# Kernel optimization log

Hardware: AMD Instinct MI355X
Metric: run time of the kernel (lower is better)

Reference implementation:

```python
import jax, jax.numpy as jnp
import numpy as np

BS, SEQ, DIM, L = 32, 256, 6, 400
NH, DM, DFF, DOUT = 2, 4, 16, 32
MAXA, ILEN = SEQ // 2 + 2, 20
THR, HW = 0.001, 2


def _layernorm(x, g, b):
    m = x.mean(-1, keepdims=True)
    v = ((x - m) ** 2).mean(-1, keepdims=True)
    return (x - m) * jax.lax.rsqrt(v + 1e-5) * g + b


def _get_max(t, ws):
    # non-overlapping window peak suppression: keep only per-window argmax value
    bs, Lt = t.shape
    nwin = Lt // ws
    w = t[:, :nwin * ws].reshape(bs, nwin, ws)
    oh = jax.nn.one_hot(jnp.argmax(w, axis=2), ws, dtype=t.dtype)
    return (w * oh).reshape(bs, nwin * ws)


def reference(x, imu_mask, imu_len, conv_w, conv_b, W_b1, b_b1, W_fc, b_fc,
              Wqkv, Wo, ln1_g, ln1_b, Wf1, bf1, Wf2, bf2, ln2_g, ln2_b,
              Wout, bout, Wd1, bd1, Wd2, bd2, Wa, ba):
    bs, seq, dim, l = x.shape
    N = bs * seq
    # --- CNN encoder: valid conv1d -> relu -> 2-bin mean pool -> (N,32,2) ---
    y = jax.lax.conv_general_dilated(x.reshape(N, dim, l), conv_w, (1,), 'VALID',
                                     dimension_numbers=('NCH', 'OIH', 'NCH'))
    y = jax.nn.relu(y + conv_b[None, :, None])  # (N,32,398)
    half = y.shape[-1] // 2
    pooled = jnp.stack([y[:, :, :half].mean(-1), y[:, :, half:2 * half].mean(-1)], -1)
    cnn_flat = pooled.reshape(N, -1)  # (N,64)
    bridge_out = jax.nn.sigmoid(cnn_flat @ W_b1 + b_b1)  # (N,4)
    # --- one-step forecasting loss -> data-dependent peaks ---
    forcast_in = bridge_out.reshape(bs, seq, DM)
    shft = jnp.pad(forcast_in, ((0, 0), (1, 0), (0, 0)))[:, :-1]
    fmask = jnp.ones_like(forcast_in).at[:, 0, :].set(0.0)
    fmask = (fmask * imu_mask[:, :, 0, 0][:, :, None]).reshape(N, DM)
    forcast = shft.reshape(N, DM) @ W_fc + b_fc
    floss = jnp.mean(jnp.square(forcast * fmask - forcast_in.reshape(N, DM) * fmask), axis=1)
    floss = floss.reshape(bs, seq)
    lmask = jnp.ones_like(floss).at[:, :2].set(0.0).at[:, -2:].set(0.0)
    floss = floss * ((floss > THR) * lmask)
    sel = _get_max(floss, 2 * HW)            # (bs,seq)
    sel2 = _get_max(sel[:, HW:], 2 * HW)     # (bs,seq-4)
    sel2 = jnp.pad(sel2, ((0, 0), (HW, 0)))
    if sel.shape[1] > sel2.shape[1]:
        sel2 = jnp.pad(sel2, ((0, 0), (0, HW)))
    seg_points = sel2 > 0
    last = jnp.clip(jnp.round(imu_len.astype(jnp.float32) / seq).astype(jnp.int32), 2, seq)
    # --- merge unit-length segments (vectorized equivalent of the while-loop) ---
    pos = jnp.arange(seq)
    point = seg_points & (pos[None] < last[:, None])
    bnd_next = jnp.pad(point, ((0, 0), (0, 1)))[:, 1:] | (pos[None] + 1 == last[:, None])
    kept = point & ~bnd_next                 # a boundary survives iff next segment len > 1
    seg_id = jnp.cumsum(kept, axis=1)
    valid_t = pos[None] < last[:, None]
    same = (seg_id[:, :, None] == seg_id[:, None, :]) & valid_t[:, :, None] & valid_t[:, None, :]
    attn_mask = jnp.where(same | jnp.eye(seq, dtype=bool)[None], 0.0, -jnp.inf)[:, None]
    # --- 1-layer post-norm transformer with block-diagonal mask ---
    hb = bridge_out.reshape(seq, bs, DM).transpose(1, 0, 2)  # faithful reshape order
    qkv = jnp.einsum('bsd,cde->cbse', hb, Wqkv)
    hd = DM // NH
    q, k, v = [t.reshape(bs, seq, NH, hd) for t in qkv]
    scores = jnp.einsum('bqhd,bkhd->bhqk', q, k) / np.sqrt(hd) + attn_mask
    attn = jax.nn.softmax(scores, axis=-1)
    ao = jnp.einsum('bhqk,bkhd->bqhd', attn, v).reshape(bs, seq, DM) @ Wo
    h1 = _layernorm(hb + ao, ln1_g, ln1_b)
    ff = jax.nn.relu(h1 @ Wf1 + bf1) @ Wf2 + bf2
    h2 = _layernorm(h1 + ff, ln2_g, ln2_b)
    tr_out = h2 @ Wout + bout                # (bs,seq,32)
    # --- per-segment atom embeddings, padded to MAXA slots ---
    n_kept = kept.sum(1)
    kp = jnp.sort(jnp.where(kept, pos[None], seq), axis=1)[:, :MAXA]
    a_idx = jnp.arange(MAXA)
    ends = jnp.where(a_idx[None] < n_kept[:, None], kp, last[:, None])
    starts = jnp.concatenate([jnp.zeros((bs, 1), ends.dtype), ends[:, :-1]], axis=1)
    atom_valid = (a_idx[None] <= n_kept[:, None]).astype(x.dtype)
    emb = jnp.take_along_axis(tr_out, jnp.clip(ends - 1, 0, seq - 1)[:, :, None], axis=1)
    atom_gen = (emb.reshape(-1, DOUT) @ Wa + ba).reshape(bs, MAXA, dim, ILEN)
    atom_gen = atom_gen * atom_valid[:, :, None, None]
    # --- per-segment nearest resample to ILEN via one batched gather ---
    xf = x.transpose(0, 2, 1, 3).reshape(bs, dim, seq * l)
    in_len = (ends - starts) * l
    idx = starts[:, :, None] * l + (jnp.arange(ILEN)[None, None] * in_len[:, :, None]) // ILEN
    idx = jnp.clip(idx, 0, seq * l - 1)
    seg_interp = xf[jnp.arange(bs)[:, None, None], :, idx]  # (bs,MAXA,ILEN,dim)
    seg_interp = seg_interp.transpose(0, 1, 3, 2) * atom_valid[:, :, None, None]
    # --- imu decoder ---
    imu_gen = (jax.nn.relu(bridge_out @ Wd1 + bd1) @ Wd2 + bd2).reshape(bs, seq, dim, l)
    return jnp.concatenate([imu_gen.ravel(), atom_gen.ravel(), seg_interp.ravel(),
                            forcast.ravel(), floss.ravel()])


def setup_inputs() -> dict:
    key = jax.random.key(0)
    ks = jax.random.split(key, 20)
    f32 = jnp.float32
    nrm = lambda k, s, sc: jax.random.normal(k, s, f32) * sc
    inp = {
        'x': nrm(ks[0], (BS, SEQ, DIM, L), 1.0),
        'imu_mask': jnp.ones((BS, SEQ, 1, 1), f32),
        'imu_len': jax.random.randint(ks[1], (BS,), SEQ * SEQ // 2, SEQ * SEQ),
        'conv_w': nrm(ks[2], (32, DIM, 3), 0.24),
        'conv_b': jnp.zeros((32,), f32),
        'W_b1': nrm(ks[3], (64, DM), 0.125),
        'b_b1': jnp.zeros((DM,), f32),
        'W_fc': nrm(ks[4], (DM, DM), 0.5),
        'b_fc': jnp.zeros((DM,), f32),
        'Wqkv': nrm(ks[5], (3, DM, DM), 0.5),
        'Wo': nrm(ks[6], (DM, DM), 0.5),
        'ln1_g': jnp.ones((DM,), f32), 'ln1_b': jnp.zeros((DM,), f32),
        'Wf1': nrm(ks[7], (DM, DFF), 0.5), 'bf1': jnp.zeros((DFF,), f32),
        'Wf2': nrm(ks[8], (DFF, DM), 0.25), 'bf2': jnp.zeros((DM,), f32),
        'ln2_g': jnp.ones((DM,), f32), 'ln2_b': jnp.zeros((DM,), f32),
        'Wout': nrm(ks[9], (DM, DOUT), 0.5), 'bout': jnp.zeros((DOUT,), f32),
        'Wd1': nrm(ks[10], (DM, 64), 0.5), 'bd1': jnp.zeros((64,), f32),
        'Wd2': nrm(ks[11], (64, DIM * L), 0.125), 'bd2': jnp.zeros((DIM * L,), f32),
        'Wa': nrm(ks[12], (DOUT, DIM * ILEN), 0.18), 'ba': jnp.zeros((DIM * ILEN,), f32),
    }
    return inp
```

## Files before the change

kernel.cpp:

```cpp
#include <hip/hip_runtime.h>
#include <hip/hip_bf16.h>
#include <math.h>

#define OFF_IMU  0
#define OFF_ATOM 19660800
#define OFF_SEG  20160000
#define OFF_FC   20659200
#define OFF_FL   20691968

#define WS_BRIDGE 0
#define WS_TR     32768
#define WS_ENDS   303104
#define WS_STARTS 307264
#define WS_NK     311424

static __device__ __forceinline__ int imin(int a, int b) { return a < b ? a : b; }
static __device__ __forceinline__ int imax(int a, int b) { return a > b ? a : b; }

typedef __attribute__((ext_vector_type(8))) short bf16x8;
typedef __attribute__((ext_vector_type(4))) float f32x4;
union AF { uint32_t u[4]; bf16x8 v; };

static __device__ __forceinline__ uint32_t pack_hilo(float x)
{
    __hip_bfloat16 h = __float2bfloat16(x);
    const float hf = __bfloat162float(h);
    __hip_bfloat16 lo = __float2bfloat16(x - hf);
    const uint32_t hb = *(const unsigned short*)&h;
    const uint32_t lb = *(const unsigned short*)&lo;
    return hb | (lb << 16);
}

__global__ __launch_bounds__(128) void k1_conv_bridge(
    const float* __restrict__ x, const float* __restrict__ conv_w,
    const float* __restrict__ conv_b, const float* __restrict__ W_b1,
    const float* __restrict__ b_b1, float* __restrict__ bridge)
{
    __shared__ __align__(16) uint32_t xsu[2][2424];
    __shared__ float pooledL[2][64];
    const int tid = threadIdx.x;
    const int n0 = blockIdx.x * 2;

    const int wv = tid >> 6;
    const int l  = tid & 63;
    const int r  = l & 15;
    const int kb = l >> 4;

    {
        const float4* xw = (const float4*)(x + (size_t)(n0 + wv) * 2400);
        uint32_t* xd = xsu[wv];
#pragma unroll
        for (int k = 0; k < 10; ++k) {
            const int i = l + k * 64;
            if (k < 9 || i < 600) {
                const float4 v = xw[i];
                const int ic = i / 100;
                const int t4 = (i - ic * 100) * 4;
                uint4 p;
                p.x = pack_hilo(v.x); p.y = pack_hilo(v.y);
                p.z = pack_hilo(v.z); p.w = pack_hilo(v.w);
                *(uint4*)&xd[ic * 404 + t4] = p;
            }
        }
        if (l < 24) xd[(l >> 2) * 404 + 400 + (l & 3)] = 0;
    }

    AF Bhi[2], Blo[2];
    float bias[2];
#pragma unroll
    for (int ot = 0; ot < 2; ++ot) {
        const float* wp = conv_w + (size_t)(r + ot * 16) * 18;
#pragma unroll
        for (int j = 0; j < 4; ++j) {
            const int k0 = kb * 8 + 2 * j, k1 = k0 + 1;
            const float w0 = (k0 < 18) ? wp[k0] : 0.0f;
            const float w1 = (k1 < 18) ? wp[k1] : 0.0f;
            const uint32_t e0 = pack_hilo(w0), e1 = pack_hilo(w1);
            Bhi[ot].u[j] = (e0 & 0xffffu) | (e1 << 16);
            Blo[ot].u[j] = (e0 >> 16) | (e1 & 0xffff0000u);
        }
        bias[ot] = conv_b[r + ot * 16];
    }

    int eoff[8];
#pragma unroll
    for (int s = 0; s < 8; ++s) {
        const int k = kb * 8 + s;
        const int ic = k / 3;
        const int dt = k - 3 * ic;
        eoff[s] = (k < 18) ? (ic * 404 + dt) : 0;
    }
    const uint32_t* ab = xsu[wv] + r;

    float p00 = 0.f, p01 = 0.f, p10 = 0.f, p11 = 0.f;

#pragma unroll
    for (int tile = 0; tile < 25; ++tile) {
        uint32_t e[8];
#pragma unroll
        for (int s = 0; s < 8; ++s) e[s] = ab[eoff[s] + tile * 16];
        AF Ahi, Alo;
#pragma unroll
        for (int j = 0; j < 4; ++j) {
            Ahi.u[j] = __builtin_amdgcn_perm(e[2 * j + 1], e[2 * j], 0x05040100u);
            Alo.u[j] = __builtin_amdgcn_perm(e[2 * j + 1], e[2 * j], 0x07060302u);
        }
        f32x4 acc0 = {0.f, 0.f, 0.f, 0.f};
        f32x4 acc1 = {0.f, 0.f, 0.f, 0.f};
        acc0 = __builtin_amdgcn_mfma_f32_16x16x32_bf16(Ahi.v, Bhi[0].v, acc0, 0, 0, 0);
        acc1 = __builtin_amdgcn_mfma_f32_16x16x32_bf16(Ahi.v, Bhi[1].v, acc1, 0, 0, 0);
        acc0 = __builtin_amdgcn_mfma_f32_16x16x32_bf16(Ahi.v, Blo[0].v, acc0, 0, 0, 0);
        acc1 = __builtin_amdgcn_mfma_f32_16x16x32_bf16(Ahi.v, Blo[1].v, acc1, 0, 0, 0);
        acc0 = __builtin_amdgcn_mfma_f32_16x16x32_bf16(Alo.v, Bhi[0].v, acc0, 0, 0, 0);
        acc1 = __builtin_amdgcn_mfma_f32_16x16x32_bf16(Alo.v, Bhi[1].v, acc1, 0, 0, 0);
#pragma unroll
        for (int reg = 0; reg < 4; ++reg) {
            const int t = tile * 16 + kb * 4 + reg;
            const float r0 = fmaxf(acc0[reg] + bias[0], 0.0f);
            const float r1 = fmaxf(acc1[reg] + bias[1], 0.0f);
            const bool h0 = t < 199;
            const bool h1 = (t >= 199) && (t < 398);
            p00 += h0 ? r0 : 0.0f;  p01 += h1 ? r0 : 0.0f;
            p10 += h0 ? r1 : 0.0f;  p11 += h1 ? r1 : 0.0f;
        }
    }

    p00 += __shfl_xor(p00, 16); p00 += __shfl_xor(p00, 32);
    p01 += __shfl_xor(p01, 16); p01 += __shfl_xor(p01, 32);
    p10 += __shfl_xor(p10, 16); p10 += __shfl_xor(p10, 32);
    p11 += __shfl_xor(p11, 16); p11 += __shfl_xor(p11, 32);

    const float inv199 = 1.0f / 199.0f;
    if (l < 16) {
        pooledL[wv][l * 2 + 0] = p00 * inv199;
        pooledL[wv][l * 2 + 1] = p01 * inv199;
        pooledL[wv][(l + 16) * 2 + 0] = p10 * inv199;
        pooledL[wv][(l + 16) * 2 + 1] = p11 * inv199;
    }

    {
        const float v = pooledL[wv][l];
        const float4 wb = *(const float4*)(W_b1 + l * 4);
        float q0 = v * wb.x, q1 = v * wb.y, q2 = v * wb.z, q3 = v * wb.w;
#pragma unroll
        for (int off = 1; off < 64; off <<= 1) {
            q0 += __shfl_xor(q0, off, 64);
            q1 += __shfl_xor(q1, off, 64);
            q2 += __shfl_xor(q2, off, 64);
            q3 += __shfl_xor(q3, off, 64);
        }
        if (l == 0) {
            float* bp = bridge + (size_t)(n0 + wv) * 4;
            bp[0] = 1.0f / (1.0f + __expf(-(q0 + b_b1[0])));
            bp[1] = 1.0f / (1.0f + __expf(-(q1 + b_b1[1])));
            bp[2] = 1.0f / (1.0f + __expf(-(q2 + b_b1[2])));
            bp[3] = 1.0f / (1.0f + __expf(-(q3 + b_b1[3])));
        }
    }
}

__global__ __launch_bounds__(256) void k234_seg_attn(
    const float* __restrict__ bridge, const float* __restrict__ imu_mask,
    const float* __restrict__ W_fc, const float* __restrict__ b_fc,
    const int* __restrict__ imu_len, float* __restrict__ out,
    int* __restrict__ ends_ws, int* __restrict__ starts_ws, int* __restrict__ nk_ws,
    const float* __restrict__ Wqkv, const float* __restrict__ Wo,
    const float* __restrict__ ln1_g, const float* __restrict__ ln1_b,
    const float* __restrict__ Wf1, const float* __restrict__ bf1,
    const float* __restrict__ Wf2, const float* __restrict__ bf2,
    const float* __restrict__ ln2_g, const float* __restrict__ ln2_b,
    const float* __restrict__ Wout, const float* __restrict__ bout,
    float* __restrict__ tr_ws)
{
    const int b = blockIdx.x >> 3;
    const int chunk = blockIdx.x & 7;
    const int tid = threadIdx.x;
    __shared__ float kv[256][8];
    __shared__ int sid[256];
    __shared__ float part[32][8][8];
    __shared__ float fl[256];
    __shared__ float sel[256];
    __shared__ float sp[256];
    __shared__ int pk[256];
    __shared__ int sc[2][256];
    __shared__ int kpl[256];

    {
        const float4 h = *(const float4*)(bridge + (size_t)(tid * 32 + b) * 4);
#pragma unroll
        for (int e = 0; e < 4; ++e) {
            kv[tid][e]     = h.x * Wqkv[16 + e] + h.y * Wqkv[20 + e] + h.z * Wqkv[24 + e] + h.w * Wqkv[28 + e];
            kv[tid][4 + e] = h.x * Wqkv[32 + e] + h.y * Wqkv[36 + e] + h.z * Wqkv[40 + e] + h.w * Wqkv[44 + e];
        }
    }

    {
        const int n = b * 256 + tid;
        float sh[4], cur[4];
#pragma unroll
        for (int j = 0; j < 4; ++j) {
            sh[j] = (tid == 0) ? 0.0f : bridge[(n - 1) * 4 + j];
            cur[j] = bridge[n * 4 + j];
        }
        const float fm = ((tid == 0) ? 0.0f : 1.0f) * imu_mask[n];
        float flv = 0.0f;
#pragma unroll
        for (int j = 0; j < 4; ++j) {
            float f = b_fc[j];
#pragma unroll
            for (int i = 0; i < 4; ++i) f = fmaf(sh[i], W_fc[i * 4 + j], f);
            out[OFF_FC + n * 4 + j] = f;
            const float d = (f - cur[j]) * fm;
            flv = fmaf(d, d, flv);
        }
        flv *= 0.25f;
        const bool lm = (tid >= 2) && (tid < 254);
        flv = (flv > 0.001f && lm) ? flv : 0.0f;
        out[OFF_FL + n] = flv;
        fl[tid] = flv;
        sp[tid] = 0.0f;
    }
    __syncthreads();

    if (tid < 64) {
        const int base = tid * 4;
        float m = fl[base]; int idx = 0;
#pragma unroll
        for (int i = 1; i < 4; ++i) { float v = fl[base + i]; if (v > m) { m = v; idx = i; } }
#pragma unroll
        for (int i = 0; i < 4; ++i) sel[base + i] = (i == idx) ? m : 0.0f;
    }
    __syncthreads();
    if (tid < 63) {
        const int base = 2 + tid * 4;
        float m = sel[base]; int idx = 0;
#pragma unroll
        for (int i = 1; i < 4; ++i) { float v = sel[base + i]; if (v > m) { m = v; idx = i; } }
        sp[base + idx] = (m > 0.0f) ? 1.0f : 0.0f;
    }
    __syncthreads();
    int last = (int)rintf((float)imu_len[b] * (1.0f / 256.0f));
    last = imin(imax(last, 2), 256);
    const int point = ((sp[tid] > 0.0f) && (tid < last)) ? 1 : 0;
    pk[tid] = point;
    __syncthreads();
    const int pnext = (tid < 255) ? pk[tid + 1] : 0;
    const int bnd = pnext | ((tid + 1 == last) ? 1 : 0);
    const int kept = (point && !bnd) ? 1 : 0;
    __syncthreads();
    sc[0][tid] = kept;
    __syncthreads();
    int src = 0;
    for (int off = 1; off < 256; off <<= 1) {
        const int v = sc[src][tid] + ((tid >= off) ? sc[src][tid - off] : 0);
        sc[src ^ 1][tid] = v;
        __syncthreads();
        src ^= 1;
    }
    const int myid = sc[src][tid];
    sid[tid] = myid;
    const int nk = sc[src][255];
    if (kept) kpl[myid - 1] = tid;
    __syncthreads();
    if (tid < 130) {
        ends_ws[b * 130 + tid] = (tid < nk) ? kpl[tid] : last;
        starts_ws[b * 130 + tid] = (tid == 0) ? 0 : ((tid - 1 < nk) ? kpl[tid - 1] : last);
    }
    if (tid == 0) nk_ws[b] = nk;

    const int lq = tid & 31;
    const int jg = tid >> 5;
    const int sq = chunk * 32 + lq;
    {
        const float4 h = *(const float4*)(bridge + (size_t)(sq * 32 + b) * 4);
        float qv[4];
#pragma unroll
        for (int e = 0; e < 4; ++e)
            qv[e] = h.x * Wqkv[e] + h.y * Wqkv[4 + e] + h.z * Wqkv[8 + e] + h.w * Wqkv[12 + e];
        const bool vs = sq < last;
        const int ms = sid[sq];
        const float isq = 0.70710678118654752f;
        float m0 = -1e30f, l0 = 0.f, a00 = 0.f, a01 = 0.f;
        float m1 = -1e30f, l1 = 0.f, a10 = 0.f, a11 = 0.f;
#pragma unroll 4
        for (int jj = 0; jj < 32; ++jj) {
            const int j = jg * 32 + jj;
            const bool allowed = (j == sq) || (vs && (j < last) && (sid[j] == ms));
            const float sc0 = (qv[0] * kv[j][0] + qv[1] * kv[j][1]) * isq;
            const float sc1 = (qv[2] * kv[j][2] + qv[3] * kv[j][3]) * isq;
            {
                const float mn = allowed ? fmaxf(m0, sc0) : m0;
                const float c = __expf(m0 - mn);
                const float e = allowed ? __expf(sc0 - mn) : 0.0f;
                l0 = l0 * c + e; a00 = a00 * c + e * kv[j][4]; a01 = a01 * c + e * kv[j][5]; m0 = mn;
            }
            {
                const float mn = allowed ? fmaxf(m1, sc1) : m1;
                const float c = __expf(m1 - mn);
                const float e = allowed ? __expf(sc1 - mn) : 0.0f;
                l1 = l1 * c + e; a10 = a10 * c + e * kv[j][6]; a11 = a11 * c + e * kv[j][7]; m1 = mn;
            }
        }
        float* pp = part[lq][jg];
        pp[0] = m0; pp[1] = l0; pp[2] = a00; pp[3] = a01;
        pp[4] = m1; pp[5] = l1; pp[6] = a10; pp[7] = a11;
    }
    __syncthreads();
    if (tid < 32) {
        const int s = chunk * 32 + tid;
        float M0 = -1e30f, L0 = 0.f, A00 = 0.f, A01 = 0.f;
        float M1 = -1e30f, L1 = 0.f, A10 = 0.f, A11 = 0.f;
#pragma unroll
        for (int p = 0; p < 8; ++p) {
            const float* pp = part[tid][p];
            {
                const float mn = fmaxf(M0, pp[0]);
                const float c0 = __expf(M0 - mn), c1 = __expf(pp[0] - mn);
                L0 = L0 * c0 + pp[1] * c1; A00 = A00 * c0 + pp[2] * c1; A01 = A01 * c0 + pp[3] * c1; M0 = mn;
            }
            {
                const float mn = fmaxf(M1, pp[4]);
                const float c0 = __expf(M1 - mn), c1 = __expf(pp[4] - mn);
                L1 = L1 * c0 + pp[5] * c1; A10 = A10 * c0 + pp[6] * c1; A11 = A11 * c0 + pp[7] * c1; M1 = mn;
            }
        }
        const float4 h = *(const float4*)(bridge + (size_t)(s * 32 + b) * 4);
        const float hb0 = h.x, hb1 = h.y, hb2 = h.z, hb3 = h.w;
        float ao[4] = {A00 / L0, A01 / L0, A10 / L1, A11 / L1};
        float x1[4];
#pragma unroll
        for (int jj = 0; jj < 4; ++jj)
            x1[jj] = ao[0] * Wo[jj] + ao[1] * Wo[4 + jj] + ao[2] * Wo[8 + jj] + ao[3] * Wo[12 + jj];
        x1[0] += hb0; x1[1] += hb1; x1[2] += hb2; x1[3] += hb3;
        float mean = 0.25f * (x1[0] + x1[1] + x1[2] + x1[3]);
        float var = 0.f;
#pragma unroll
        for (int i = 0; i < 4; ++i) { float d = x1[i] - mean; var += d * d; }
        var *= 0.25f;
        const float rs1 = rsqrtf(var + 1e-5f);
        float h1v[4];
#pragma unroll
        for (int i = 0; i < 4; ++i) h1v[i] = (x1[i] - mean) * rs1 * ln1_g[i] + ln1_b[i];
        float o2[4] = {bf2[0], bf2[1], bf2[2], bf2[3]};
#pragma unroll
        for (int kk = 0; kk < 16; ++kk) {
            float t = bf1[kk];
#pragma unroll
            for (int i = 0; i < 4; ++i) t = fmaf(h1v[i], Wf1[i * 16 + kk], t);
            t = fmaxf(t, 0.0f);
#pragma unroll
            for (int jj = 0; jj < 4; ++jj) o2[jj] = fmaf(t, Wf2[kk * 4 + jj], o2[jj]);
        }
        float x2[4];
#pragma unroll
        for (int i = 0; i < 4; ++i) x2[i] = h1v[i] + o2[i];
        float mean2 = 0.25f * (x2[0] + x2[1] + x2[2] + x2[3]);
        float var2 = 0.f;
#pragma unroll
        for (int i = 0; i < 4; ++i) { float d = x2[i] - mean2; var2 += d * d; }
        var2 *= 0.25f;
        const float rs2 = rsqrtf(var2 + 1e-5f);
        float h2v[4];
#pragma unroll
        for (int i = 0; i < 4; ++i) h2v[i] = (x2[i] - mean2) * rs2 * ln2_g[i] + ln2_b[i];
        float* tp = tr_ws + ((size_t)(b * 256 + s)) * 32;
#pragma unroll
        for (int mm = 0; mm < 32; ++mm)
            tp[mm] = bout[mm] + h2v[0] * Wout[mm] + h2v[1] * Wout[32 + mm]
                   + h2v[2] * Wout[64 + mm] + h2v[3] * Wout[96 + mm];
    }
}

__global__ __launch_bounds__(128) void k5_atoms(
    const float* __restrict__ x, const float* __restrict__ tr_ws,
    const int* __restrict__ ends_ws, const int* __restrict__ starts_ws,
    const int* __restrict__ nk_ws,
    const float* __restrict__ Wa, const float* __restrict__ ba,
    float* __restrict__ out)
{
    const int a = blockIdx.x;
    const int b = blockIdx.y;
    const int tid = threadIdx.x;
    __shared__ float emb[32];
    const int e = ends_ws[b * 130 + a];
    const int st = starts_ws[b * 130 + a];
    const int nk = nk_ws[b];
    const float valid = (a <= nk) ? 1.0f : 0.0f;
    const int ec = imin(imax(e - 1, 0), 255);
    if (tid < 32) emb[tid] = tr_ws[((size_t)(b * 256 + ec)) * 32 + tid];
    __syncthreads();
    if (tid < 120) {
        float v = ba[tid];
#pragma unroll
        for (int f = 0; f < 32; ++f) v = fmaf(emb[f], Wa[f * 120 + tid], v);
        out[OFF_ATOM + ((size_t)(b * 130 + a)) * 120 + tid] = v * valid;
        const int d = tid / 20, i = tid % 20;
        const int ilen = (e - st) * 400;
        int idx = st * 400 + (i * ilen) / 20;
        idx = imin(imax(idx, 0), 102399);
        const int si = idx / 400, ti = idx % 400;
        const float px = x[(((size_t)b * 256 + si) * 6 + d) * 400 + ti];
        out[OFF_SEG + ((size_t)(b * 130 + a)) * 120 + tid] = px * valid;
    }
}

__global__ __launch_bounds__(256) void k6_imu(
    const float* __restrict__ bridge, const float* __restrict__ Wd1,
    const float* __restrict__ bd1, const float* __restrict__ Wd2,
    const float* __restrict__ bd2, float* __restrict__ out)
{
    __shared__ float hl[64 * 32];
    const int n0 = blockIdx.x * 32;
    const int mb = blockIdx.y;
    const int tid = threadIdx.x;
    for (int e = tid; e < 2048; e += 256) {
        const int f = e >> 5, i = e & 31;
        const float4 br = *(const float4*)(bridge + (size_t)(n0 + i) * 4);
        const float v = bd1[f] + br.x * Wd1[f] + br.y * Wd1[64 + f]
                      + br.z * Wd1[128 + f] + br.w * Wd1[192 + f];
        hl[f * 32 + i] = fmaxf(v, 0.0f);
    }
    __syncthreads();
    const int gm = tid & 63, gn = tid >> 6;
    const int m0 = mb * 256 + gm * 4;
    if (m0 >= 2400) return;
    float acc[8][4];
#pragma unroll
    for (int r = 0; r < 8; ++r)
#pragma unroll
        for (int c = 0; c < 4; ++c) acc[r][c] = 0.f;
#pragma unroll 4
    for (int f = 0; f < 64; ++f) {
        const float4 w4 = *(const float4*)&Wd2[(size_t)f * 2400 + m0];
        const float4 h0 = *(const float4*)&hl[f * 32 + gn * 8];
        const float4 h1 = *(const float4*)&hl[f * 32 + gn * 8 + 4];
        const float hv[8] = {h0.x, h0.y, h0.z, h0.w, h1.x, h1.y, h1.z, h1.w};
        const float wv[4] = {w4.x, w4.y, w4.z, w4.w};
#pragma unroll
        for (int r = 0; r < 8; ++r)
#pragma unroll
            for (int c = 0; c < 4; ++c) acc[r][c] = fmaf(hv[r], wv[c], acc[r][c]);
    }
    const float4 bb = *(const float4*)&bd2[m0];
#pragma unroll
    for (int r = 0; r < 8; ++r) {
        float4 o;
        o.x = acc[r][0] + bb.x; o.y = acc[r][1] + bb.y;
        o.z = acc[r][2] + bb.z; o.w = acc[r][3] + bb.w;
        *(float4*)&out[OFF_IMU + (size_t)(n0 + gn * 8 + r) * 2400 + m0] = o;
    }
}

extern "C" void kernel_launch(void* const* d_in, const int* in_sizes, int n_in,
                              void* d_out, int out_size, void* d_ws, size_t ws_size,
                              hipStream_t stream)
{
    const float* x        = (const float*)d_in[0];
    const float* imu_mask = (const float*)d_in[1];
    const int*   imu_len  = (const int*)  d_in[2];
    const float* conv_w   = (const float*)d_in[3];
    const float* conv_b   = (const float*)d_in[4];
    const float* W_b1     = (const float*)d_in[5];
    const float* b_b1     = (const float*)d_in[6];
    const float* W_fc     = (const float*)d_in[7];
    const float* b_fc     = (const float*)d_in[8];
    const float* Wqkv     = (const float*)d_in[9];
    const float* Wo       = (const float*)d_in[10];
    const float* ln1_g    = (const float*)d_in[11];
    const float* ln1_b    = (const float*)d_in[12];
    const float* Wf1      = (const float*)d_in[13];
    const float* bf1      = (const float*)d_in[14];
    const float* Wf2      = (const float*)d_in[15];
    const float* bf2      = (const float*)d_in[16];
    const float* ln2_g    = (const float*)d_in[17];
    const float* ln2_b    = (const float*)d_in[18];
    const float* Wout     = (const float*)d_in[19];
    const float* bout     = (const float*)d_in[20];
    const float* Wd1      = (const float*)d_in[21];
    const float* bd1      = (const float*)d_in[22];
    const float* Wd2      = (const float*)d_in[23];
    const float* bd2      = (const float*)d_in[24];
    const float* Wa       = (const float*)d_in[25];
    const float* ba       = (const float*)d_in[26];

    float* out = (float*)d_out;
    float* wsf = (float*)d_ws;
    int*   wsi = (int*)d_ws;

    float* bridge = wsf + WS_BRIDGE;
    float* tr_ws  = wsf + WS_TR;
    int* ends   = wsi + WS_ENDS;
    int* starts = wsi + WS_STARTS;
    int* nk     = wsi + WS_NK;

    k1_conv_bridge<<<4096, 128, 0, stream>>>(x, conv_w, conv_b, W_b1, b_b1, bridge);
    k234_seg_attn<<<256, 256, 0, stream>>>(bridge, imu_mask, W_fc, b_fc, imu_len,
                                           out, ends, starts, nk,
                                           Wqkv, Wo, ln1_g, ln1_b, Wf1, bf1,
                                           Wf2, bf2, ln2_g, ln2_b, Wout, bout, tr_ws);
    k5_atoms<<<dim3(130, 32), 128, 0, stream>>>(x, tr_ws, ends, starts, nk, Wa, ba, out);
    k6_imu<<<dim3(256, 10), 256, 0, stream>>>(bridge, Wd1, bd1, Wd2, bd2, out);
}
```

Baseline: 112.5 us.

## Build im2col tile in shared memory and split one sample across two waves

The conv kernel now gives each 128-thread block a single sample and writes an im2col (unrolled-window) copy of the input into shared memory, using row stride 21 to limit bank conflicts. Each MFMA A-fragment then becomes eight contiguous LDS reads instead of eight scattered offset loads. The two waves split the 25 time tiles (13 each, with the overhang masked) and combine their pooled partial sums through shared memory after a barrier, and the grid doubles to 8192 blocks. In exchange, each input element is written three times to LDS, zero-padding writes and two block barriers are added, and more LDS per block may lower occupancy.

Result: slower. 141.5 us (+25.8%).

```diff
diff --git a/kernel.cpp b/kernel.cpp
--- a/kernel.cpp
+++ b/kernel.cpp
@@ -31,38 +31,57 @@
     return hb | (lb << 16);
 }
 
+#define IMS 21
+#define IMROWS 417
+
 __global__ __launch_bounds__(128) void k1_conv_bridge(
     const float* __restrict__ x, const float* __restrict__ conv_w,
     const float* __restrict__ conv_b, const float* __restrict__ W_b1,
     const float* __restrict__ b_b1, float* __restrict__ bridge)
 {
-    __shared__ __align__(16) uint32_t xsu[2][2424];
-    __shared__ float pooledL[2][64];
+    __shared__ uint32_t xd[IMROWS * IMS];
+    __shared__ float part[2][4][16];
     const int tid = threadIdx.x;
-    const int n0 = blockIdx.x * 2;
+    const int n = blockIdx.x;
 
     const int wv = tid >> 6;
     const int l  = tid & 63;
     const int r  = l & 15;
     const int kb = l >> 4;
 
+    for (int i = tid; i < 1200; i += 128) {
+        const int row = i / 3;
+        xd[row * IMS + 18 + (i - row * 3)] = 0;
+    }
+    for (int i = tid; i < 357; i += 128)
+        xd[400 * IMS + i] = 0;
+    if (tid < 18) {
+        int row, col;
+        if (tid < 6)       { row = 398; col = tid * 3 + 2; }
+        else               { const int j = tid - 6; row = 399;
+                             col = (j >> 1) * 3 + 1 + (j & 1); }
+        xd[row * IMS + col] = 0;
+    }
+
     {
-        const float4* xw = (const float4*)(x + (size_t)(n0 + wv) * 2400);
-        uint32_t* xd = xsu[wv];
-#pragma unroll
-        for (int k = 0; k < 10; ++k) {
-            const int i = l + k * 64;
-            if (k < 9 || i < 600) {
-                const float4 v = xw[i];
-                const int ic = i / 100;
-                const int t4 = (i - ic * 100) * 4;
-                uint4 p;
-                p.x = pack_hilo(v.x); p.y = pack_hilo(v.y);
-                p.z = pack_hilo(v.z); p.w = pack_hilo(v.w);
-                *(uint4*)&xd[ic * 404 + t4] = p;
+        const float4* xw = (const float4*)(x + (size_t)n * 2400);
+        for (int i = tid; i < 600; i += 128) {
+            const float4 v = xw[i];
+            const int ic = i / 100;
+            const int t4 = (i - ic * 100) * 4;
+            const int k3 = ic * 3;
+            const float vv[4] = {v.x, v.y, v.z, v.w};
+#pragma unroll
+            for (int e = 0; e < 4; ++e) {
+                const int T = t4 + e;
+                const uint32_t u = pack_hilo(vv[e]);
+#pragma unroll
+                for (int dt = 0; dt < 3; ++dt) {
+                    const int row = T - dt;
+                    if (row >= 0) xd[row * IMS + k3 + dt] = u;
+                }
             }
         }
-        if (l < 24) xd[(l >> 2) * 404 + 400 + (l & 3)] = 0;
     }
 
     AF Bhi[2], Blo[2];
@@ -82,23 +101,17 @@
         bias[ot] = conv_b[r + ot * 16];
     }
 
-    int eoff[8];
-#pragma unroll
-    for (int s = 0; s < 8; ++s) {
-        const int k = kb * 8 + s;
-        const int ic = k / 3;
-        const int dt = k - 3 * ic;
-        eoff[s] = (k < 18) ? (ic * 404 + dt) : 0;
-    }
-    const uint32_t* ab = xsu[wv] + r;
-
+    __syncthreads();
+
+    const int tileoff = wv * 13;
+    const uint32_t* ab = xd + (size_t)(tileoff * 16 + r) * IMS + kb * 8;
     float p00 = 0.f, p01 = 0.f, p10 = 0.f, p11 = 0.f;
 
 #pragma unroll
-    for (int tile = 0; tile < 25; ++tile) {
+    for (int tt = 0; tt < 13; ++tt) {
         uint32_t e[8];
 #pragma unroll
-        for (int s = 0; s < 8; ++s) e[s] = ab[eoff[s] + tile * 16];
+        for (int s = 0; s < 8; ++s) e[s] = ab[tt * (16 * IMS) + s];
         AF Ahi, Alo;
 #pragma unroll
         for (int j = 0; j < 4; ++j) {
@@ -115,7 +128,7 @@
         acc1 = __builtin_amdgcn_mfma_f32_16x16x32_bf16(Alo.v, Bhi[1].v, acc1, 0, 0, 0);
 #pragma unroll
         for (int reg = 0; reg < 4; ++reg) {
-            const int t = tile * 16 + kb * 4 + reg;
+            const int t = (tileoff + tt) * 16 + kb * 4 + reg;
             const float r0 = fmaxf(acc0[reg] + bias[0], 0.0f);
             const float r1 = fmaxf(acc1[reg] + bias[1], 0.0f);
             const bool h0 = t < 199;
@@ -130,17 +143,19 @@
     p10 += __shfl_xor(p10, 16); p10 += __shfl_xor(p10, 32);
     p11 += __shfl_xor(p11, 16); p11 += __shfl_xor(p11, 32);
 
-    const float inv199 = 1.0f / 199.0f;
     if (l < 16) {
-        pooledL[wv][l * 2 + 0] = p00 * inv199;
-        pooledL[wv][l * 2 + 1] = p01 * inv199;
-        pooledL[wv][(l + 16) * 2 + 0] = p10 * inv199;
-        pooledL[wv][(l + 16) * 2 + 1] = p11 * inv199;
-    }
-
-    {
-        const float v = pooledL[wv][l];
-        const float4 wb = *(const float4*)(W_b1 + l * 4);
+        part[wv][0][l] = p00;  part[wv][1][l] = p01;
+        part[wv][2][l] = p10;  part[wv][3][l] = p11;
+    }
+    __syncthreads();
+
+    if (tid < 64) {
+        const int f = tid;
+        const int oc = f >> 1, h = f & 1;
+        const int idx = (oc < 16) ? h : (2 + h);
+        const int c = oc & 15;
+        const float v = (part[0][idx][c] + part[1][idx][c]) * (1.0f / 199.0f);
+        const float4 wb = *(const float4*)(W_b1 + f * 4);
         float q0 = v * wb.x, q1 = v * wb.y, q2 = v * wb.z, q3 = v * wb.w;
 #pragma unroll
         for (int off = 1; off < 64; off <<= 1) {
@@ -149,8 +164,8 @@
             q2 += __shfl_xor(q2, off, 64);
             q3 += __shfl_xor(q3, off, 64);
         }
-        if (l == 0) {
-            float* bp = bridge + (size_t)(n0 + wv) * 4;
+        if (f == 0) {
+            float* bp = bridge + (size_t)n * 4;
             bp[0] = 1.0f / (1.0f + __expf(-(q0 + b_b1[0])));
             bp[1] = 1.0f / (1.0f + __expf(-(q1 + b_b1[1])));
             bp[2] = 1.0f / (1.0f + __expf(-(q2 + b_b1[2])));
@@ -493,7 +508,7 @@
     int* starts = wsi + WS_STARTS;
     int* nk     = wsi + WS_NK;
 
-    k1_conv_bridge<<<4096, 128, 0, stream>>>(x, conv_w, conv_b, W_b1, b_b1, bridge);
+    k1_conv_bridge<<<8192, 128, 0, stream>>>(x, conv_w, conv_b, W_b1, b_b1, bridge);
     k234_seg_attn<<<256, 256, 0, stream>>>(bridge, imu_mask, W_fc, b_fc, imu_len,
                                            out, ends, starts, nk,
                                            Wqkv, Wo, ln1_g, ln1_b, Wf1, bf1,
```
